# Kernel tuning notes

Hardware: AMD Instinct MI355X
Metric: run time of the kernel (lower is better)

The kernel has to match this reference:

```python
import jax, jax.numpy as jnp
import numpy as np

ALPHA = 1.702
LIMIT = 7.0

E, H, D = 16, 1024, 1024  # num_experts, hidden_size, expert_dim
B, S = 1, 2048


def setup_inputs() -> dict:
    key = jax.random.key(0)
    ks = jax.random.split(key, 6)
    return {
        "hidden_states": jax.random.normal(ks[0], (B, S, H), dtype=jnp.float32),
        "routing_weights": jax.random.uniform(ks[1], (B * S, E), dtype=jnp.float32),
        "gate_up_proj": jax.random.normal(ks[2], (E, H, 2 * D), dtype=jnp.float32) * 0.02,
        "gate_up_proj_bias": jax.random.normal(ks[3], (E, 2 * D), dtype=jnp.float32) * 0.02,
        "down_proj": jax.random.normal(ks[4], (E, D, H), dtype=jnp.float32) * 0.02,
        "down_proj_bias": jax.random.normal(ks[5], (E, H), dtype=jnp.float32) * 0.02,
    }


def reference(hidden_states, routing_weights, gate_up_proj, gate_up_proj_bias,
              down_proj, down_proj_bias):
    batch = hidden_states.shape[0]
    hs = hidden_states.reshape(-1, H)  # [T, H], T = B*S
    # dense per-expert gate_up projection: [E, T, 2D]
    gate_up = jnp.einsum('th,ehd->etd', hs, gate_up_proj) + gate_up_proj_bias[:, None, :]
    gate = gate_up[..., ::2]   # [E, T, D]
    up = gate_up[..., 1::2]    # [E, T, D]
    gate = jnp.minimum(gate, LIMIT)
    up = jnp.clip(up, -LIMIT, LIMIT)
    glu = gate * jax.nn.sigmoid(gate * ALPHA)
    # down projection: [E, T, H]
    next_states = jnp.einsum('etd,edh->eth', (up + 1.0) * glu, down_proj)
    next_states = next_states + down_proj_bias[:, None, :]
    # weighted sum over experts with routing_weights [T, E]
    out = jnp.einsum('eth,te->th', next_states, routing_weights)
    return out.reshape(batch, -1, H)
```

## Files before the change

### kernel.cpp

```cpp
#include <hip/hip_runtime.h>
#include <hip/hip_bf16.h>
#include <cstdint>
#include <cstddef>

#define E_     16
#define H_     1024
#define D_     1024
#define T_     2048
#define TWO_D  2048
#define KFLAT  (E_ * D_)

typedef float  f32x4  __attribute__((ext_vector_type(4)));
typedef short  bf16x8 __attribute__((ext_vector_type(8)));

static __device__ __forceinline__ unsigned short f2bf(float f) {
  union { float f; unsigned u; } v; v.f = f;
  unsigned u = v.u;
  unsigned r = (u + 0x7FFFu + ((u >> 16) & 1u)) >> 16;
  return (unsigned short)r;
}

static __device__ __forceinline__ void gload16(const void* g, void* l) {
  __builtin_amdgcn_global_load_lds(
      (const __attribute__((address_space(1))) void*)g,
      (__attribute__((address_space(3))) void*)l, 16, 0, 0);
}

__global__ void k_trans_gu(const float* __restrict__ gu,
                           unsigned short* __restrict__ wg,
                           unsigned short* __restrict__ wu) {
  __shared__ float tile[64][65];
  const int e  = blockIdx.z;
  const int h0 = blockIdx.y * 64;
  const int c0 = blockIdx.x * 64;
  const int tid = threadIdx.x;
  const float* src = gu + (size_t)e * H_ * TWO_D;
#pragma unroll
  for (int i = 0; i < 16; ++i) {
    int lin = tid + i * 256;
    int hr = lin >> 6, c = lin & 63;
    tile[hr][c] = src[(size_t)(h0 + hr) * TWO_D + c0 + c];
  }
  __syncthreads();
  const int d0 = c0 >> 1;
#pragma unroll
  for (int i = 0; i < 4; ++i) {
    int lin = tid + i * 256;
    int dg = lin >> 5, hp = lin & 31;
    int h = hp * 2;
    ushort2 o = make_ushort2(f2bf(tile[h][dg * 2]), f2bf(tile[h + 1][dg * 2]));
    *(ushort2*)&wg[(((size_t)e << 10) + d0 + dg) * H_ + h0 + h] = o;
  }
#pragma unroll
  for (int i = 0; i < 4; ++i) {
    int lin = tid + i * 256;
    int dg = lin >> 5, hp = lin & 31;
    int h = hp * 2;
    ushort2 o = make_ushort2(f2bf(tile[h][dg * 2 + 1]), f2bf(tile[h + 1][dg * 2 + 1]));
    *(ushort2*)&wu[(((size_t)e << 10) + d0 + dg) * H_ + h0 + h] = o;
  }
}

__global__ void k_trans_dn(const float* __restrict__ dn,
                           unsigned short* __restrict__ wd) {
  __shared__ float tile[64][65];
  const int e  = blockIdx.z;
  const int d0 = blockIdx.y * 64;
  const int h0 = blockIdx.x * 64;
  const int tid = threadIdx.x;
  const float* src = dn + (size_t)e * D_ * H_;
#pragma unroll
  for (int i = 0; i < 16; ++i) {
    int lin = tid + i * 256;
    int dr = lin >> 6, hc = lin & 63;
    tile[dr][hc] = src[(size_t)(d0 + dr) * H_ + h0 + hc];
  }
  __syncthreads();
#pragma unroll
  for (int i = 0; i < 8; ++i) {
    int lin = tid + i * 256;
    int hr = lin >> 5, dp = lin & 31;
    ushort2 o = make_ushort2(f2bf(tile[dp * 2][hr]), f2bf(tile[dp * 2 + 1][hr]));
    *(ushort2*)&wd[(size_t)(h0 + hr) * KFLAT + (e << 10) + d0 + dp * 2] = o;
  }
}

__global__ void k_cvt_hs(const float* __restrict__ hs, unsigned short* __restrict__ hb) {
  int idx = blockIdx.x * blockDim.x + threadIdx.x;
  float4 v = ((const float4*)hs)[idx];
  ushort4 o;
  o.x = f2bf(v.x); o.y = f2bf(v.y); o.z = f2bf(v.z); o.w = f2bf(v.w);
  ((ushort4*)hb)[idx] = o;
}

__global__ void k_bias_out(const float* __restrict__ rw, const float* __restrict__ db,
                           float* __restrict__ out) {
  int idx = blockIdx.x * blockDim.x + threadIdx.x;
  int t = idx >> 10, h = idx & 1023;
  const float* r = rw + t * E_;
  float acc = 0.f;
#pragma unroll
  for (int e = 0; e < E_; ++e) acc += r[e] * db[(e << 10) + h];
  out[idx] = acc;
}

__global__ void __launch_bounds__(256)
k_gemm1(const unsigned short* __restrict__ hb,
        const unsigned short* __restrict__ wg,
        const unsigned short* __restrict__ wu,
        const float* __restrict__ gub,
        const float* __restrict__ rw,
        unsigned short* __restrict__ act) {
  __shared__ __align__(16) short lsA[128 * 64];
  __shared__ __align__(16) short lsB[128 * 64];
  const int e  = blockIdx.z;
  const int t0 = blockIdx.y * 128;
  const int d0 = blockIdx.x * 64;
  const int tid  = threadIdx.x;
  const int lane = tid & 63;
  const int w    = tid >> 6;

  f32x4 acc[2][8];
#pragma unroll
  for (int mi = 0; mi < 2; ++mi)
#pragma unroll
    for (int nf = 0; nf < 8; ++nf) acc[mi][nf] = (f32x4)0.f;

  for (int kt = 0; kt < H_ / 64; ++kt) {
    const int k0 = kt * 64;
#pragma unroll
    for (int i = 0; i < 4; ++i) {
      int lin = tid + i * 256;
      int row = lin >> 3, ch = lin & 7;
      gload16(hb + (size_t)(t0 + row) * H_ + k0 + ch * 8, &lsA[lin * 8]);
    }
#pragma unroll
    for (int i = 0; i < 4; ++i) {
      int lin = tid + i * 256;
      int row = lin >> 3, ch = lin & 7;
      const unsigned short* gb = (row < 64)
          ? wg + (((size_t)e << 10) + d0 + row) * H_ + k0 + ch * 8
          : wu + (((size_t)e << 10) + d0 + (row - 64)) * H_ + k0 + ch * 8;
      gload16(gb, &lsB[lin * 8]);
    }
    __syncthreads();
#pragma unroll
    for (int ks = 0; ks < 2; ++ks) {
      const int koff = ks * 32 + ((lane >> 4) << 3);
      bf16x8 af[2], bfr[8];
#pragma unroll
      for (int mi = 0; mi < 2; ++mi)
        af[mi] = *(const bf16x8*)&lsA[((w * 32 + mi * 16 + (lane & 15)) << 6) + koff];
#pragma unroll
      for (int nf = 0; nf < 8; ++nf)
        bfr[nf] = *(const bf16x8*)&lsB[((nf * 16 + (lane & 15)) << 6) + koff];
#pragma unroll
      for (int mi = 0; mi < 2; ++mi)
#pragma unroll
        for (int nf = 0; nf < 8; ++nf)
          acc[mi][nf] = __builtin_amdgcn_mfma_f32_16x16x32_bf16(af[mi], bfr[nf], acc[mi][nf], 0, 0, 0);
    }
    __syncthreads();
  }

  const int col = lane & 15;
#pragma unroll
  for (int mi = 0; mi < 2; ++mi) {
#pragma unroll
    for (int rr = 0; rr < 4; ++rr) {
      const int t = t0 + w * 32 + mi * 16 + ((lane >> 4) << 2) + rr;
      const float r = rw[t * E_ + e];
#pragma unroll
      for (int nf = 0; nf < 4; ++nf) {
        const int d = d0 + nf * 16 + col;
        float g = acc[mi][nf][rr]     + gub[e * TWO_D + 2 * d];
        float u = acc[mi][nf + 4][rr] + gub[e * TWO_D + 2 * d + 1];
        g = fminf(g, 7.0f);
        u = fminf(fmaxf(u, -7.0f), 7.0f);
        float glu = g / (1.0f + __expf(-1.702f * g));
        float a = (u + 1.0f) * glu * r;
        act[(size_t)t * KFLAT + (e << 10) + d] = f2bf(a);
      }
    }
  }
}

__global__ void __launch_bounds__(256)
k_gemm2(const unsigned short* __restrict__ act,
        const unsigned short* __restrict__ wd,
        float* __restrict__ out) {
  __shared__ __align__(16) short lsA[128 * 64];
  __shared__ __align__(16) short lsB[128 * 64];
  const int ks_blk = blockIdx.z;
  const int t0 = blockIdx.y * 128;
  const int h0 = blockIdx.x * 128;
  const int tid  = threadIdx.x;
  const int lane = tid & 63;
  const int w    = tid >> 6;
  const int wm = w >> 1, wn = w & 1;

  f32x4 acc[4][4];
#pragma unroll
  for (int mi = 0; mi < 4; ++mi)
#pragma unroll
    for (int nf = 0; nf < 4; ++nf) acc[mi][nf] = (f32x4)0.f;

  const int kbeg = ks_blk * (KFLAT / 4);
  for (int kt = 0; kt < (KFLAT / 4) / 64; ++kt) {
    const int k0 = kbeg + kt * 64;
#pragma unroll
    for (int i = 0; i < 4; ++i) {
      int lin = tid + i * 256;
      int row = lin >> 3, ch = lin & 7;
      gload16(act + (size_t)(t0 + row) * KFLAT + k0 + ch * 8, &lsA[lin * 8]);
    }
#pragma unroll
    for (int i = 0; i < 4; ++i) {
      int lin = tid + i * 256;
      int row = lin >> 3, ch = lin & 7;
      gload16(wd + (size_t)(h0 + row) * KFLAT + k0 + ch * 8, &lsB[lin * 8]);
    }
    __syncthreads();
#pragma unroll
    for (int ks = 0; ks < 2; ++ks) {
      const int koff = ks * 32 + ((lane >> 4) << 3);
      bf16x8 af[4], bfr[4];
#pragma unroll
      for (int mi = 0; mi < 4; ++mi)
        af[mi] = *(const bf16x8*)&lsA[((wm * 64 + mi * 16 + (lane & 15)) << 6) + koff];
#pragma unroll
      for (int nf = 0; nf < 4; ++nf)
        bfr[nf] = *(const bf16x8*)&lsB[((wn * 64 + nf * 16 + (lane & 15)) << 6) + koff];
#pragma unroll
      for (int mi = 0; mi < 4; ++mi)
#pragma unroll
        for (int nf = 0; nf < 4; ++nf)
          acc[mi][nf] = __builtin_amdgcn_mfma_f32_16x16x32_bf16(af[mi], bfr[nf], acc[mi][nf], 0, 0, 0);
    }
    __syncthreads();
  }

  const int col = lane & 15;
#pragma unroll
  for (int mi = 0; mi < 4; ++mi) {
#pragma unroll
    for (int rr = 0; rr < 4; ++rr) {
      const int t = t0 + wm * 64 + mi * 16 + ((lane >> 4) << 2) + rr;
#pragma unroll
      for (int nf = 0; nf < 4; ++nf) {
        const int h = h0 + wn * 64 + nf * 16 + col;
        atomicAdd(&out[(size_t)t * H_ + h], acc[mi][nf][rr]);
      }
    }
  }
}

extern "C" void kernel_launch(void* const* d_in, const int* in_sizes, int n_in,
                              void* d_out, int out_size, void* d_ws, size_t ws_size,
                              hipStream_t stream) {
  const float* hs  = (const float*)d_in[0];
  const float* rw  = (const float*)d_in[1];
  const float* gup = (const float*)d_in[2];
  const float* gub = (const float*)d_in[3];
  const float* dnp = (const float*)d_in[4];
  const float* dnb = (const float*)d_in[5];
  float* out = (float*)d_out;

  char* ws = (char*)d_ws;
  unsigned short* hb  = (unsigned short*)(ws);
  unsigned short* wg  = (unsigned short*)(ws + (4UL   << 20));
  unsigned short* wu  = (unsigned short*)(ws + (36UL  << 20));
  unsigned short* wd  = (unsigned short*)(ws + (68UL  << 20));
  unsigned short* act = (unsigned short*)(ws + (100UL << 20));

  k_cvt_hs  <<<(T_ * H_ / 4) / 256, 256, 0, stream>>>(hs, hb);
  k_trans_gu<<<dim3(TWO_D / 64, H_ / 64, E_), 256, 0, stream>>>(gup, wg, wu);
  k_trans_dn<<<dim3(H_ / 64, D_ / 64, E_),    256, 0, stream>>>(dnp, wd);
  k_bias_out<<<(T_ * H_) / 256, 256, 0, stream>>>(rw, dnb, out);
  k_gemm1   <<<dim3(D_ / 64, T_ / 128, E_),   256, 0, stream>>>(hb, wg, wu, gub, rw, act);
  k_gemm2   <<<dim3(H_ / 128, T_ / 128, 4),   256, 0, stream>>>(act, wd, out);
}
```

Baseline: 626.0 us.

## Double-buffer LDS tiles, XOR-swizzle LDS layout, and use 2x2 warp tiling in gemm1

Both GEMM kernels now keep two LDS buffers and prefetch the next K tile while the current one feeds the MFMAs, so only one barrier is needed per iteration. LDS rows are stored with an XOR swizzle on the 16-byte chunk index to avoid bank conflicts when fragments are read. gemm1 also switches from a 4x1 to a 2x2 warp layout, with gate and up rows interleaved in 16-row groups so each warp holds matching gate/up fragments. LDS use per block doubles, which may lower occupancy.

Measured after the change: 573.7 us. 8.4% less time.

```diff
diff --git a/kernel.cpp b/kernel.cpp
--- a/kernel.cpp
+++ b/kernel.cpp
@@ -111,75 +111,84 @@
         const float* __restrict__ gub,
         const float* __restrict__ rw,
         unsigned short* __restrict__ act) {
-  __shared__ __align__(16) short lsA[128 * 64];
-  __shared__ __align__(16) short lsB[128 * 64];
+  __shared__ __align__(16) short lsA[2][128 * 64];
+  __shared__ __align__(16) short lsB[2][128 * 64];
   const int e  = blockIdx.z;
   const int t0 = blockIdx.y * 128;
   const int d0 = blockIdx.x * 64;
   const int tid  = threadIdx.x;
   const int lane = tid & 63;
   const int w    = tid >> 6;
-
-  f32x4 acc[2][8];
-#pragma unroll
-  for (int mi = 0; mi < 2; ++mi)
-#pragma unroll
-    for (int nf = 0; nf < 8; ++nf) acc[mi][nf] = (f32x4)0.f;
-
+  const int wm = w >> 1, wn = w & 1;
+  const int lo = lane & 15, hi = lane >> 4;
+
+  f32x4 acc[4][4];
+#pragma unroll
+  for (int mi = 0; mi < 4; ++mi)
+#pragma unroll
+    for (int nf = 0; nf < 4; ++nf) acc[mi][nf] = (f32x4)0.f;
+
+#define G1_STAGE(buf, k0)                                                      \
+  {                                                                            \
+    _Pragma("unroll")                                                          \
+    for (int i = 0; i < 4; ++i) {                                              \
+      int lin = tid + i * 256; int row = lin >> 3, ch = lin & 7;               \
+      int sch = ch ^ (row & 7);                                                \
+      gload16(hb + (size_t)(t0 + row) * H_ + (k0) + sch * 8,                   \
+              &lsA[buf][lin * 8]);                                             \
+    }                                                                          \
+    _Pragma("unroll")                                                          \
+    for (int i = 0; i < 4; ++i) {                                              \
+      int lin = tid + i * 256; int row = lin >> 3, ch = lin & 7;               \
+      int sch = ch ^ (row & 7);                                                \
+      int dl = ((row >> 5) << 4) + (row & 15);                                 \
+      const unsigned short* bp = ((row >> 4) & 1) ? wu : wg;                   \
+      gload16(bp + (((size_t)e << 10) + d0 + dl) * H_ + (k0) + sch * 8,        \
+              &lsB[buf][lin * 8]);                                             \
+    }                                                                          \
+  }
+
+  G1_STAGE(0, 0);
+  __syncthreads();
+  int cur = 0;
   for (int kt = 0; kt < H_ / 64; ++kt) {
-    const int k0 = kt * 64;
-#pragma unroll
-    for (int i = 0; i < 4; ++i) {
-      int lin = tid + i * 256;
-      int row = lin >> 3, ch = lin & 7;
-      gload16(hb + (size_t)(t0 + row) * H_ + k0 + ch * 8, &lsA[lin * 8]);
-    }
-#pragma unroll
-    for (int i = 0; i < 4; ++i) {
-      int lin = tid + i * 256;
-      int row = lin >> 3, ch = lin & 7;
-      const unsigned short* gb = (row < 64)
-          ? wg + (((size_t)e << 10) + d0 + row) * H_ + k0 + ch * 8
-          : wu + (((size_t)e << 10) + d0 + (row - 64)) * H_ + k0 + ch * 8;
-      gload16(gb, &lsB[lin * 8]);
-    }
-    __syncthreads();
+    if (kt + 1 < H_ / 64) G1_STAGE(cur ^ 1, (kt + 1) * 64);
 #pragma unroll
     for (int ks = 0; ks < 2; ++ks) {
-      const int koff = ks * 32 + ((lane >> 4) << 3);
-      bf16x8 af[2], bfr[8];
-#pragma unroll
-      for (int mi = 0; mi < 2; ++mi)
-        af[mi] = *(const bf16x8*)&lsA[((w * 32 + mi * 16 + (lane & 15)) << 6) + koff];
-#pragma unroll
-      for (int nf = 0; nf < 8; ++nf)
-        bfr[nf] = *(const bf16x8*)&lsB[((nf * 16 + (lane & 15)) << 6) + koff];
-#pragma unroll
-      for (int mi = 0; mi < 2; ++mi)
-#pragma unroll
-        for (int nf = 0; nf < 8; ++nf)
+      const int cb = (((ks << 2) | hi) ^ (lo & 7)) << 3;
+      bf16x8 af[4], bfr[4];
+#pragma unroll
+      for (int mi = 0; mi < 4; ++mi)
+        af[mi] = *(const bf16x8*)&lsA[cur][(wm * 64 + mi * 16 + lo) * 64 + cb];
+#pragma unroll
+      for (int nf = 0; nf < 4; ++nf)
+        bfr[nf] = *(const bf16x8*)&lsB[cur][(wn * 64 + nf * 16 + lo) * 64 + cb];
+#pragma unroll
+      for (int mi = 0; mi < 4; ++mi)
+#pragma unroll
+        for (int nf = 0; nf < 4; ++nf)
           acc[mi][nf] = __builtin_amdgcn_mfma_f32_16x16x32_bf16(af[mi], bfr[nf], acc[mi][nf], 0, 0, 0);
     }
     __syncthreads();
-  }
-
-  const int col = lane & 15;
-#pragma unroll
-  for (int mi = 0; mi < 2; ++mi) {
+    cur ^= 1;
+  }
+#undef G1_STAGE
+
+#pragma unroll
+  for (int mi = 0; mi < 4; ++mi) {
 #pragma unroll
     for (int rr = 0; rr < 4; ++rr) {
-      const int t = t0 + w * 32 + mi * 16 + ((lane >> 4) << 2) + rr;
+      const int t = t0 + wm * 64 + mi * 16 + hi * 4 + rr;
       const float r = rw[t * E_ + e];
 #pragma unroll
-      for (int nf = 0; nf < 4; ++nf) {
-        const int d = d0 + nf * 16 + col;
-        float g = acc[mi][nf][rr]     + gub[e * TWO_D + 2 * d];
-        float u = acc[mi][nf + 4][rr] + gub[e * TWO_D + 2 * d + 1];
+      for (int j = 0; j < 2; ++j) {
+        const int d = d0 + wn * 32 + j * 16 + lo;
+        float g = acc[mi][2 * j][rr]     + gub[e * TWO_D + 2 * d];
+        float u = acc[mi][2 * j + 1][rr] + gub[e * TWO_D + 2 * d + 1];
         g = fminf(g, 7.0f);
         u = fminf(fmaxf(u, -7.0f), 7.0f);
         float glu = g / (1.0f + __expf(-1.702f * g));
-        float a = (u + 1.0f) * glu * r;
-        act[(size_t)t * KFLAT + (e << 10) + d] = f2bf(a);
+        act[(size_t)t * KFLAT + (e << 10) + d] = f2bf((u + 1.0f) * glu * r);
       }
     }
   }
@@ -189,8 +198,8 @@
 k_gemm2(const unsigned short* __restrict__ act,
         const unsigned short* __restrict__ wd,
         float* __restrict__ out) {
-  __shared__ __align__(16) short lsA[128 * 64];
-  __shared__ __align__(16) short lsB[128 * 64];
+  __shared__ __align__(16) short lsA[2][128 * 64];
+  __shared__ __align__(16) short lsB[2][128 * 64];
   const int ks_blk = blockIdx.z;
   const int t0 = blockIdx.y * 128;
   const int h0 = blockIdx.x * 128;
@@ -198,6 +207,7 @@
   const int lane = tid & 63;
   const int w    = tid >> 6;
   const int wm = w >> 1, wn = w & 1;
+  const int lo = lane & 15, hi = lane >> 4;
 
   f32x4 acc[4][4];
 #pragma unroll
@@ -205,32 +215,41 @@
 #pragma unroll
     for (int nf = 0; nf < 4; ++nf) acc[mi][nf] = (f32x4)0.f;
 
+#define G2_STAGE(buf, k0)                                                      \
+  {                                                                            \
+    _Pragma("unroll")                                                          \
+    for (int i = 0; i < 4; ++i) {                                              \
+      int lin = tid + i * 256; int row = lin >> 3, ch = lin & 7;               \
+      int sch = ch ^ (row & 7);                                                \
+      gload16(act + (size_t)(t0 + row) * KFLAT + (k0) + sch * 8,               \
+              &lsA[buf][lin * 8]);                                             \
+    }                                                                          \
+    _Pragma("unroll")                                                          \
+    for (int i = 0; i < 4; ++i) {                                              \
+      int lin = tid + i * 256; int row = lin >> 3, ch = lin & 7;               \
+      int sch = ch ^ (row & 7);                                                \
+      gload16(wd + (size_t)(h0 + row) * KFLAT + (k0) + sch * 8,                \
+              &lsB[buf][lin * 8]);                                             \
+    }                                                                          \
+  }
+
   const int kbeg = ks_blk * (KFLAT / 4);
-  for (int kt = 0; kt < (KFLAT / 4) / 64; ++kt) {
-    const int k0 = kbeg + kt * 64;
-#pragma unroll
-    for (int i = 0; i < 4; ++i) {
-      int lin = tid + i * 256;
-      int row = lin >> 3, ch = lin & 7;
-      gload16(act + (size_t)(t0 + row) * KFLAT + k0 + ch * 8, &lsA[lin * 8]);
-    }
-#pragma unroll
-    for (int i = 0; i < 4; ++i) {
-      int lin = tid + i * 256;
-      int row = lin >> 3, ch = lin & 7;
-      gload16(wd + (size_t)(h0 + row) * KFLAT + k0 + ch * 8, &lsB[lin * 8]);
-    }
-    __syncthreads();
+  const int NKT  = (KFLAT / 4) / 64;
+  G2_STAGE(0, kbeg);
+  __syncthreads();
+  int cur = 0;
+  for (int kt = 0; kt < NKT; ++kt) {
+    if (kt + 1 < NKT) G2_STAGE(cur ^ 1, kbeg + (kt + 1) * 64);
 #pragma unroll
     for (int ks = 0; ks < 2; ++ks) {
-      const int koff = ks * 32 + ((lane >> 4) << 3);
+      const int cb = (((ks << 2) | hi) ^ (lo & 7)) << 3;
       bf16x8 af[4], bfr[4];
 #pragma unroll
       for (int mi = 0; mi < 4; ++mi)
-        af[mi] = *(const bf16x8*)&lsA[((wm * 64 + mi * 16 + (lane & 15)) << 6) + koff];
+        af[mi] = *(const bf16x8*)&lsA[cur][(wm * 64 + mi * 16 + lo) * 64 + cb];
 #pragma unroll
       for (int nf = 0; nf < 4; ++nf)
-        bfr[nf] = *(const bf16x8*)&lsB[((wn * 64 + nf * 16 + (lane & 15)) << 6) + koff];
+        bfr[nf] = *(const bf16x8*)&lsB[cur][(wn * 64 + nf * 16 + lo) * 64 + cb];
 #pragma unroll
       for (int mi = 0; mi < 4; ++mi)
 #pragma unroll
@@ -238,17 +257,18 @@
           acc[mi][nf] = __builtin_amdgcn_mfma_f32_16x16x32_bf16(af[mi], bfr[nf], acc[mi][nf], 0, 0, 0);
     }
     __syncthreads();
-  }
-
-  const int col = lane & 15;
+    cur ^= 1;
+  }
+#undef G2_STAGE
+
 #pragma unroll
   for (int mi = 0; mi < 4; ++mi) {
 #pragma unroll
     for (int rr = 0; rr < 4; ++rr) {
-      const int t = t0 + wm * 64 + mi * 16 + ((lane >> 4) << 2) + rr;
+      const int t = t0 + wm * 64 + mi * 16 + hi * 4 + rr;
 #pragma unroll
       for (int nf = 0; nf < 4; ++nf) {
-        const int h = h0 + wn * 64 + nf * 16 + col;
+        const int h = h0 + wn * 64 + nf * 16 + lo;
         atomicAdd(&out[(size_t)t * H_ + h], acc[mi][nf][rr]);
       }
     }
```
